# Kernel tuning notes

Hardware: AMD Instinct MI355X
Metric: run time of the kernel (lower is better)

The kernel has to match this reference:

```python
import jax, jax.numpy as jnp
import numpy as np

S = 4096      # total packed sequence length (8 images x 512 patches)
D = 1152      # hidden_dim
H = 16        # num_heads
HD = D // H   # head_dim = 72
MLPD = 4304   # mlp_dim
EPS = 1e-5


def setup_inputs() -> dict:
    key = jax.random.key(0)
    ks = jax.random.split(key, 16)
    f32 = jnp.float32
    w = lambda k, shp: (jax.random.normal(k, shp, f32) * 0.02)
    hidden_states = jax.random.normal(ks[0], (S, D), f32)
    cu_seqlens = (jnp.arange(9, dtype=jnp.int32) * (S // 8))  # [0,512,...,4096]
    angles = jax.random.uniform(ks[1], (S, HD // 2), f32, 0.0, 2.0 * np.pi)
    rope_cos = jnp.cos(angles)
    rope_sin = jnp.sin(angles)
    return {
        "hidden_states": hidden_states,
        "cu_seqlens": cu_seqlens,
        "rope_cos": rope_cos,
        "rope_sin": rope_sin,
        "norm0_scale": jnp.ones((D,), f32),
        "norm0_bias": jnp.zeros((D,), f32),
        "wqkv_w": w(ks[2], (D, 3 * D)),
        "wqkv_b": jnp.zeros((3 * D,), f32),
        "wo_w": w(ks[3], (D, D)),
        "wo_b": jnp.zeros((D,), f32),
        "norm1_scale": jnp.ones((D,), f32),
        "norm1_bias": jnp.zeros((D,), f32),
        "fc0_w": w(ks[4], (D, MLPD)),
        "fc0_b": jnp.zeros((MLPD,), f32),
        "fc1_w": w(ks[5], (MLPD, D)),
        "fc1_b": jnp.zeros((D,), f32),
    }


def _layernorm(x, scale, bias):
    m = jnp.mean(x, axis=-1, keepdims=True)
    v = jnp.mean(jnp.square(x - m), axis=-1, keepdims=True)
    return (x - m) * jax.lax.rsqrt(v + EPS) * scale + bias


def _rope(x, cos, sin):
    # x: (S, H, HD). Complex multiply (x0 + i x1) * (cos + i sin) in real form.
    xr = x.reshape(S, H, HD // 2, 2)
    x0, x1 = xr[..., 0], xr[..., 1]
    c = cos[:, None, :]  # (S, 1, HD/2) broadcast over heads
    s = sin[:, None, :]
    o0 = x0 * c - x1 * s
    o1 = x0 * s + x1 * c
    return jnp.stack([o0, o1], axis=-1).reshape(S, H, HD)


def _block_diag_bias(cu_seqlens):
    positions = jnp.arange(S)
    starts, ends = cu_seqlens[:-1], cu_seqlens[1:]
    in_seg = (positions[:, None] >= starts[None, :]) & (positions[:, None] < ends[None, :])
    seg = jnp.argmax(in_seg.astype(jnp.int32), axis=-1)  # (S,)
    same = seg[:, None] == seg[None, :]
    return jnp.where(same, 0.0, jnp.finfo(jnp.float32).min)  # (S, S)


def reference(hidden_states, cu_seqlens, rope_cos, rope_sin,
              norm0_scale, norm0_bias, wqkv_w, wqkv_b, wo_w, wo_b,
              norm1_scale, norm1_bias, fc0_w, fc0_b, fc1_w, fc1_b):
    # pre-norm attention block
    x = _layernorm(hidden_states, norm0_scale, norm0_bias)
    qkv = (x @ wqkv_w + wqkv_b).reshape(S, 3, H, HD)
    q, k, v = qkv[:, 0], qkv[:, 1], qkv[:, 2]
    q = _rope(q, rope_cos, rope_sin)
    k = _rope(k, rope_cos, rope_sin)
    bias = _block_diag_bias(cu_seqlens)  # (S, S)
    scale = HD ** -0.5
    scores = jnp.einsum('shd,thd->hst', q, k) * scale + bias[None, :, :]
    probs = jax.nn.softmax(scores, axis=-1)
    attn = jnp.einsum('hst,thd->shd', probs, v).reshape(S, D)
    attn = attn @ wo_w + wo_b
    h = hidden_states + attn
    # pre-norm MLP block
    y = _layernorm(h, norm1_scale, norm1_bias)
    y = jax.nn.gelu(y @ fc0_w + fc0_b) @ fc1_w + fc1_b
    return h + y
```

## Files before the change

### kernel.cpp

```cpp
#include <hip/hip_runtime.h>


#define DEV __device__ __forceinline__

typedef __attribute__((ext_vector_type(8))) short short8;
typedef __attribute__((ext_vector_type(4))) float f32x4;

typedef const void __attribute__((address_space(1))) gvoid;
typedef void __attribute__((address_space(3))) lvoid;

DEV ushort f2bf(float f) {
  union { float f; unsigned u; } x; x.f = f;
  unsigned r = (x.u + 0x7FFFu + ((x.u >> 16) & 1u)) >> 16;
  return (ushort)r;
}

DEV float bf2f(ushort u) {
  union { unsigned u; float f; } x; x.u = (unsigned)u << 16;
  return x.f;
}

DEV void gload_lds16(const void* g, void* l) {
  __builtin_amdgcn_global_load_lds((gvoid*)g, (lvoid*)l, 16, 0, 0);
}

DEV f32x4 mfma16(short8 a, short8 b, f32x4 c) {
  return __builtin_amdgcn_mfma_f32_16x16x32_bf16(a, b, c, 0, 0, 0);
}

DEV float gelu_tanh(float x) {
  float x3 = x * x * x;
  return 0.5f * x * (1.f + tanhf(0.7978845608f * (x + 0.044715f * x3)));
}

__global__ void wconv_t(const float* __restrict__ src, ushort* __restrict__ dst,
                        int K, int N, int NP, int KP) {
  __shared__ float tile[32][33];
  const int k0 = blockIdx.x * 32, n0 = blockIdx.y * 32;
  const int tx = threadIdx.x & 31, ty = threadIdx.x >> 5;
#pragma unroll
  for (int i = 0; i < 4; ++i) {
    int r = ty + i * 8;
    float v = 0.f;
    if (k0 + r < K && n0 + tx < N) v = src[(size_t)(k0 + r) * N + n0 + tx];
    tile[tx][r] = v;
  }
  __syncthreads();
#pragma unroll
  for (int i = 0; i < 4; ++i) {
    int r = ty + i * 8;
    dst[(size_t)(n0 + r) * KP + k0 + tx] = f2bf(tile[r][tx]);
  }
}

__global__ __launch_bounds__(256) void ln_bf16(const float* __restrict__ x,
                                               const float* __restrict__ sc,
                                               const float* __restrict__ bi,
                                               ushort* __restrict__ out) {
  const int row = blockIdx.x, tid = threadIdx.x;
  const float* xr = x + (size_t)row * 1152;
  const int n = (tid < 128) ? 5 : 4;
  float vals[5];
  float s = 0.f, s2 = 0.f;
#pragma unroll
  for (int i = 0; i < 5; ++i) {
    if (i < n) { float v = xr[tid + i * 256]; vals[i] = v; s += v; s2 += v * v; }
  }
#pragma unroll
  for (int off = 32; off; off >>= 1) { s += __shfl_xor(s, off); s2 += __shfl_xor(s2, off); }
  __shared__ float rs[4], rs2[4];
  if ((tid & 63) == 0) { rs[tid >> 6] = s; rs2[tid >> 6] = s2; }
  __syncthreads();
  s = rs[0] + rs[1] + rs[2] + rs[3];
  s2 = rs2[0] + rs2[1] + rs2[2] + rs2[3];
  const float mean = s * (1.f / 1152.f);
  const float var = s2 * (1.f / 1152.f) - mean * mean;
  const float rstd = rsqrtf(var + 1e-5f);
  ushort* orow = out + (size_t)row * 1152;
  for (int i = 0; i < n; ++i) {
    int c = tid + i * 256;
    orow[c] = f2bf((vals[i] - mean) * rstd * sc[c] + bi[c]);
  }
}

#define BAR __builtin_amdgcn_s_barrier()
#define LGKM0 do { asm volatile("s_waitcnt lgkmcnt(0)" ::: "memory"); \
                   __builtin_amdgcn_sched_barrier(0); } while (0)
#define VM6 do { asm volatile("s_waitcnt vmcnt(6)" ::: "memory"); \
                 __builtin_amdgcn_sched_barrier(0); } while (0)
#define MMQ(AF, BF, MB, NB)                                                   \
  do {                                                                        \
    __builtin_amdgcn_s_setprio(1);                                            \
    _Pragma("unroll") for (int mf = 0; mf < 4; ++mf)                          \
      _Pragma("unroll") for (int nf = 0; nf < 2; ++nf) {                      \
        acc[(MB) + mf][(NB) + nf] =                                           \
            mfma16(AF[mf][0], BF[nf][0], acc[(MB) + mf][(NB) + nf]);          \
        acc[(MB) + mf][(NB) + nf] =                                           \
            mfma16(AF[mf][1], BF[nf][1], acc[(MB) + mf][(NB) + nf]);          \
      }                                                                       \
    __builtin_amdgcn_s_setprio(0);                                            \
  } while (0)

template <int EPI>
__global__ __launch_bounds__(512, 2) void gemmT(
    const ushort* __restrict__ A, const ushort* __restrict__ Bt,
    const float* __restrict__ bias, const float* __restrict__ resid,
    float* __restrict__ outf, ushort* __restrict__ outh,
    int N, int K, int NT, int n_valid) {
  __shared__ ushort lA[2][256 * 64];
  __shared__ ushort lB[2][256 * 64];
  const int tid = threadIdx.x;
  const int lane = tid & 63, wave = tid >> 6;
  const int l15 = lane & 15, lg = lane >> 4;
  const int wr = wave >> 2, wc = wave & 3;

  const int nx = gridDim.x, ny = gridDim.y;
  const int nwg = nx * ny * gridDim.z;
  int flat = (blockIdx.z * ny + blockIdx.y) * nx + blockIdx.x;
  flat = (flat & 7) * (nwg >> 3) + (flat >> 3);
  const int bx = flat % nx;
  const int rem = flat / nx;
  const int by = rem % ny;
  const int bz = rem / ny;
  const int m0 = by * 256, n0 = bx * 256;
  const int k0 = bz * NT * 64;

  const int rb8 = tid >> 3;
  const int swz = ((tid & 7) ^ (rb8 & 7)) * 8;
  const ushort* Ag = A + (size_t)m0 * K + k0 + swz;
  const ushort* Bg = Bt + (size_t)n0 * K + k0 + swz;
  const int rB = (rb8 & 31) + ((rb8 >> 5) << 6);
  const int rBw = (wave & 3) * 8 + (wave >> 2) * 64;

  auto stA = [&](int b, int u, int t) {
#pragma unroll
    for (int j = 0; j < 2; ++j) {
      const int r = u * 64 + rb8 + j * 128;
      gload_lds16(Ag + (size_t)r * K + t * 64,
                  &lA[b][(u * 64 + wave * 8 + j * 128) * 64]);
    }
  };
  auto stB = [&](int b, int c, int t) {
#pragma unroll
    for (int j = 0; j < 2; ++j) {
      const int r = rB + c * 32 + j * 128;
      gload_lds16(Bg + (size_t)r * K + t * 64,
                  &lB[b][(rBw + c * 32 + j * 128) * 64]);
    }
  };

  const int arow = wr * 128 + l15;
  const int brow = wc * 64 + l15;
  const int cp0 = ((0 + lg) ^ (l15 & 7)) * 8;
  const int cp1 = ((4 + lg) ^ (l15 & 7)) * 8;
  auto rdA = [&](int b, int half, short8 (&a)[4][2]) {
#pragma unroll
    for (int mf = 0; mf < 4; ++mf) {
      const ushort* p = &lA[b][(arow + half * 64 + mf * 16) * 64];
      a[mf][0] = *(const short8*)(p + cp0);
      a[mf][1] = *(const short8*)(p + cp1);
    }
  };
  auto rdB = [&](int b, int h, short8 (&bb)[2][2]) {
#pragma unroll
    for (int nf = 0; nf < 2; ++nf) {
      const ushort* p = &lB[b][(brow + h * 32 + nf * 16) * 64];
      bb[nf][0] = *(const short8*)(p + cp0);
      bb[nf][1] = *(const short8*)(p + cp1);
    }
  };

  f32x4 acc[8][4] = {};
  short8 aL[4][2], aH[4][2], b01[2][2], b23[2][2];

  stA(0, 0, 0); stB(0, 0, 0); stA(0, 1, 0); stB(0, 1, 0);
  stA(1, 0, 1); stB(1, 0, 1); stA(1, 1, 1); stB(1, 1, 1);
  asm volatile("s_waitcnt vmcnt(8)" ::: "memory");
  BAR;
  rdA(0, 0, aL); rdB(0, 0, b01);

  const int NIT = NT >> 1;
  for (int it = 0; it < NIT; ++it) {
    const int tn0 = 2 * it + 2, tn1 = 2 * it + 3;
    const bool more = (it + 1 < NIT);
    rdB(0, 1, b23); if (more) stA(0, 0, tn0);
    BAR; LGKM0; MMQ(aL, b01, 0, 0); BAR;
    rdA(0, 1, aH); if (more) stB(0, 0, tn0);
    BAR; LGKM0; MMQ(aL, b23, 0, 2); BAR;
    if (more) stA(0, 1, tn0);
    BAR; LGKM0; MMQ(aH, b01, 4, 0); VM6; BAR;
    rdA(1, 0, aL); rdB(1, 0, b01); if (more) stB(0, 1, tn0);
    BAR; LGKM0; MMQ(aH, b23, 4, 2); BAR;
    rdB(1, 1, b23); if (more) stA(1, 0, tn1);
    BAR; LGKM0; MMQ(aL, b01, 0, 0); BAR;
    rdA(1, 1, aH); if (more) stB(1, 0, tn1);
    BAR; LGKM0; MMQ(aL, b23, 0, 2); BAR;
    if (more) stA(1, 1, tn1);
    BAR; LGKM0; MMQ(aH, b01, 4, 0); VM6; BAR;
    rdA(0, 0, aL); rdB(0, 0, b01); if (more) stB(1, 1, tn1);
    BAR; LGKM0; MMQ(aH, b23, 4, 2); BAR;
  }

  float* outp = outf;
  if constexpr (EPI == 0) outp = outf + (size_t)bz * 4096 * 1152;
#pragma unroll
  for (int nf = 0; nf < 4; ++nf) {
    const int col = n0 + wc * 64 + nf * 16 + l15;
    if (col >= n_valid) continue;
    const float bv = (EPI != 0) ? bias[col] : 0.f;
#pragma unroll
    for (int mf = 0; mf < 8; ++mf) {
#pragma unroll
      for (int r = 0; r < 4; ++r) {
        const int row = m0 + wr * 128 + mf * 16 + lg * 4 + r;
        const size_t idx = (size_t)row * N + col;
        const float v = acc[mf][nf][r] + bv;
        if constexpr (EPI == 0) outp[idx] = v;
        else if constexpr (EPI == 1) outf[idx] = resid[idx] + v;
        else if constexpr (EPI == 2) outh[idx] = f2bf(gelu_tanh(v));
        else outh[idx] = f2bf(v);
      }
    }
  }
}

__global__ __launch_bounds__(256) void ksum_reduce(
    const float* __restrict__ hb, const float* __restrict__ bias,
    const float* __restrict__ p0, const float* __restrict__ p1,
    float* __restrict__ out) {
  const f32x4* hb4 = (const f32x4*)hb;
  const f32x4* b4 = (const f32x4*)bias;
  const f32x4* p04 = (const f32x4*)p0;
  const f32x4* p14 = (const f32x4*)p1;
  f32x4* o4 = (f32x4*)out;
  const int total = 4096 * 288;
  for (int i = blockIdx.x * 256 + threadIdx.x; i < total; i += gridDim.x * 256)
    o4[i] = hb4[i] + b4[i % 288] + p04[i] + p14[i];
}

__global__ __launch_bounds__(256) void rope_pack(
    const ushort* __restrict__ qkv,
    const float* __restrict__ cosp, const float* __restrict__ sinp,
    ushort* __restrict__ qp, ushort* __restrict__ kp) {
  const int t = blockIdx.x * 256 + threadIdx.x;
  const int c = t % 12;
  const int hs = t / 12;
  const int h = hs & 15;
  const int s = hs >> 4;
  const size_t dst = ((size_t)h * 4096 + s) * 96 + c * 8;
  if (c >= 9) {
    short8 z = {};
    *(short8*)(qp + dst) = z;
    *(short8*)(kp + dst) = z;
    return;
  }
  const size_t base = (size_t)s * 3456 + h * 72 + c * 8;
  const short8 qv = *(const short8*)(qkv + base);
  const short8 kv = *(const short8*)(qkv + base + 1152);
  const f32x4 cs = *(const f32x4*)(cosp + s * 36 + c * 4);
  const f32x4 sn = *(const f32x4*)(sinp + s * 36 + c * 4);
  short8 qo, ko;
#pragma unroll
  for (int j = 0; j < 4; ++j) {
    const float q0 = bf2f((ushort)qv[2 * j]), q1 = bf2f((ushort)qv[2 * j + 1]);
    const float k0 = bf2f((ushort)kv[2 * j]), k1 = bf2f((ushort)kv[2 * j + 1]);
    qo[2 * j] = (short)f2bf((q0 * cs[j] - q1 * sn[j]) * 0.1178511302f);
    qo[2 * j + 1] = (short)f2bf((q0 * sn[j] + q1 * cs[j]) * 0.1178511302f);
    ko[2 * j] = (short)f2bf(k0 * cs[j] - k1 * sn[j]);
    ko[2 * j + 1] = (short)f2bf(k0 * sn[j] + k1 * cs[j]);
  }
  *(short8*)(qp + dst) = qo;
  *(short8*)(kp + dst) = ko;
}

__global__ void v_pack(const ushort* __restrict__ qkv, ushort* __restrict__ vt) {
  __shared__ ushort lv[96][64];
  const int b = blockIdx.x;
  const int h = b >> 6;
  const int s0 = (b & 63) << 6;
  const int tid = threadIdx.x;
#pragma unroll
  for (int it = 0; it < 24; ++it) {
    int idx = tid + it * 256;
    int d = idx % 96, sl = idx / 96;
    lv[d][sl] = (d < 72) ? qkv[(size_t)(s0 + sl) * 3456 + 2304 + h * 72 + d] : (ushort)0;
  }
  __syncthreads();
#pragma unroll
  for (int it = 0; it < 24; ++it) {
    int idx = tid + it * 256;
    int d = idx >> 6, sl = idx & 63;
    vt[((size_t)h * 96 + d) * 4096 + s0 + sl] = lv[d][sl];
  }
}

__global__ __launch_bounds__(256) void attn_kernel(
    const ushort* __restrict__ qp, const ushort* __restrict__ kp,
    const ushort* __restrict__ vt, ushort* __restrict__ attn_out) {
  __shared__ ushort lp[4][16 * 32];
  const int tid = threadIdx.x, lane = tid & 63, wave = tid >> 6;
  const int l15 = lane & 15, lg = lane >> 4;
  const int b = blockIdx.x;
  const int h = b >> 6;
  const int rem = b & 63;
  const int seg = rem >> 3, qt = rem & 7;
  const int q0 = seg * 512 + qt * 64 + wave * 16;

  short8 aq[3];
  const ushort* qrow = qp + ((size_t)h * 4096 + q0 + l15) * 96 + lg * 8;
  aq[0] = *(const short8*)(qrow);
  aq[1] = *(const short8*)(qrow + 32);
  aq[2] = *(const short8*)(qrow + 64);

  f32x4 oacc[5] = {};
  float mrow[4] = {-1e30f, -1e30f, -1e30f, -1e30f};
  float srow[4] = {0.f, 0.f, 0.f, 0.f};

  const ushort* kbase = kp + ((size_t)h * 4096 + seg * 512) * 96;
  const ushort* vbase = vt + (size_t)h * 96 * 4096 + seg * 512;
  ushort* lpw = lp[wave];

  for (int kc = 0; kc < 16; ++kc) {
    f32x4 sc[2] = {};
#pragma unroll
    for (int n = 0; n < 2; ++n) {
      const ushort* krow = kbase + (size_t)(kc * 32 + n * 16 + l15) * 96 + lg * 8;
#pragma unroll
      for (int c = 0; c < 3; ++c) {
        short8 kb = *(const short8*)(krow + c * 32);
        sc[n] = mfma16(aq[c], kb, sc[n]);
      }
    }
    float corr[4];
#pragma unroll
    for (int j = 0; j < 4; ++j) {
      float v = fmaxf(sc[0][j], sc[1][j]);
      v = fmaxf(v, __shfl_xor(v, 1));
      v = fmaxf(v, __shfl_xor(v, 2));
      v = fmaxf(v, __shfl_xor(v, 4));
      v = fmaxf(v, __shfl_xor(v, 8));
      float mn = fmaxf(mrow[j], v);
      corr[j] = __expf(mrow[j] - mn);
      mrow[j] = mn;
    }
    float p0[4], p1[4];
#pragma unroll
    for (int j = 0; j < 4; ++j) {
      p0[j] = __expf(sc[0][j] - mrow[j]);
      p1[j] = __expf(sc[1][j] - mrow[j]);
      float ps = p0[j] + p1[j];
      ps += __shfl_xor(ps, 1);
      ps += __shfl_xor(ps, 2);
      ps += __shfl_xor(ps, 4);
      ps += __shfl_xor(ps, 8);
      srow[j] = srow[j] * corr[j] + ps;
    }
#pragma unroll
    for (int n = 0; n < 5; ++n)
#pragma unroll
      for (int j = 0; j < 4; ++j)
        oacc[n][j] *= corr[j];
#pragma unroll
    for (int j = 0; j < 4; ++j) {
      int row = lg * 4 + j;
      lpw[row * 32 + l15] = f2bf(p0[j]);
      lpw[row * 32 + 16 + l15] = f2bf(p1[j]);
    }
    __syncthreads();
    short8 pa = *(const short8*)&lpw[l15 * 32 + lg * 8];
    const ushort* vrow = vbase + kc * 32 + lg * 8;
#pragma unroll
    for (int n = 0; n < 5; ++n) {
      short8 vb = *(const short8*)(vrow + (size_t)(n * 16 + l15) * 4096);
      oacc[n] = mfma16(pa, vb, oacc[n]);
    }
    __syncthreads();
  }
#pragma unroll
  for (int j = 0; j < 4; ++j) {
    float inv = 1.f / srow[j];
    int row = q0 + lg * 4 + j;
#pragma unroll
    for (int n = 0; n < 5; ++n) {
      int col = n * 16 + l15;
      if (col < 72)
        attn_out[(size_t)row * 1152 + h * 72 + col] = f2bf(oacc[n][j] * inv);
    }
  }
}

extern "C" void kernel_launch(void* const* d_in, const int* in_sizes, int n_in,
                              void* d_out, int out_size, void* d_ws, size_t ws_size,
                              hipStream_t stream) {
  (void)in_sizes; (void)n_in; (void)out_size;
  const float* hidden = (const float*)d_in[0];
  const float* ropec = (const float*)d_in[2];
  const float* ropes = (const float*)d_in[3];
  const float* n0s = (const float*)d_in[4];
  const float* n0b = (const float*)d_in[5];
  const float* wqkv = (const float*)d_in[6];
  const float* bqkv = (const float*)d_in[7];
  const float* wo = (const float*)d_in[8];
  const float* bo = (const float*)d_in[9];
  const float* n1s = (const float*)d_in[10];
  const float* n1b = (const float*)d_in[11];
  const float* wfc0 = (const float*)d_in[12];
  const float* bfc0 = (const float*)d_in[13];
  const float* wfc1 = (const float*)d_in[14];
  const float* bfc1 = (const float*)d_in[15];
  float* out = (float*)d_out;

  char* ws = (char*)d_ws;
  ushort* x_bf   = (ushort*)(ws + 0);
  ushort* wqkv_t = (ushort*)(ws + 9437184);
  ushort* wo_t   = (ushort*)(ws + 17694720);
  ushort* fc0_t  = (ushort*)(ws + 20643840);
  ushort* fc1_t  = (ushort*)(ws + 30670848);
  ushort* qkv_bf = (ushort*)(ws + 41811968);
  ushort* mid    = (ushort*)(ws + 41811968);
  ushort* q_pad  = (ushort*)(ws + 77463552);
  ushort* k_pad  = (ushort*)(ws + 90046464);
  ushort* vt     = (ushort*)(ws + 102629376);
  float*  pbuf   = (float*)(ws + 77463552);
  ushort* attn   = (ushort*)(ws + 115212288);
  float*  hbuf   = (float*)(ws + 124649472);
  ushort* yln    = (ushort*)(ws + 143523840);
  if (ws_size < 152961024) return;

  wconv_t<<<dim3(36, 112), 256, 0, stream>>>(wqkv, wqkv_t, 1152, 3456, 3584, 1152);
  wconv_t<<<dim3(36, 40), 256, 0, stream>>>(wo, wo_t, 1152, 1152, 1280, 1152);
  wconv_t<<<dim3(36, 136), 256, 0, stream>>>(wfc0, fc0_t, 1152, 4304, 4352, 1152);
  wconv_t<<<dim3(136, 40), 256, 0, stream>>>(wfc1, fc1_t, 4304, 1152, 1280, 4352);

  ln_bf16<<<4096, 256, 0, stream>>>(hidden, n0s, n0b, x_bf);

  gemmT<3><<<dim3(14, 16), 512, 0, stream>>>(x_bf, wqkv_t, bqkv, nullptr, nullptr, qkv_bf,
                                             3456, 1152, 18, 3456);
  rope_pack<<<3072, 256, 0, stream>>>(qkv_bf, ropec, ropes, q_pad, k_pad);
  v_pack<<<1024, 256, 0, stream>>>(qkv_bf, vt);

  attn_kernel<<<1024, 256, 0, stream>>>(q_pad, k_pad, vt, attn);

  gemmT<1><<<dim3(5, 16), 512, 0, stream>>>(attn, wo_t, bo, hidden, hbuf, nullptr,
                                            1152, 1152, 18, 1152);
  ln_bf16<<<4096, 256, 0, stream>>>(hbuf, n1s, n1b, yln);

  gemmT<2><<<dim3(17, 16), 512, 0, stream>>>(yln, fc0_t, bfc0, nullptr, nullptr, mid,
                                             4352, 1152, 18, 4304);
  gemmT<0><<<dim3(5, 16, 2), 512, 0, stream>>>(mid, fc1_t, nullptr, nullptr, pbuf, nullptr,
                                               1152, 4352, 34, 1152);
  ksum_reduce<<<2048, 256, 0, stream>>>(hbuf, bfc1, pbuf, pbuf + (size_t)4096 * 1152, out);
}
```

Baseline: 401.3 us.

## Add smaller-tile GEMM kernels for out-proj and MLP layers

Adds two new GEMM kernels. gemmR uses 128x256 tiles, K-step 32 and a 4-buffer LDS pipeline three stages deep; gemm2 uses 128x128 tiles with double buffering. They replace the large-tile gemmT for the output projection, fc0 and split-K fc1. With fewer, larger tiles the old launches left many CUs idle (80 or 272 workgroups), so the smaller tiles are meant to fill the GPU better and cut N-padding waste by shrinking the padded wo/fc1 widths to 1152. The cost is less data reuse per tile and more barriers.

```diff
diff --git a/kernel.cpp b/kernel.cpp
--- a/kernel.cpp
+++ b/kernel.cpp
@@ -224,6 +224,223 @@
   }
 }
 
+template <int EPI>
+__global__ __launch_bounds__(512, 2) void gemmR(
+    const ushort* __restrict__ A, const ushort* __restrict__ Bt,
+    const float* __restrict__ bias, const float* __restrict__ resid,
+    float* __restrict__ outf, ushort* __restrict__ outh,
+    int N, int K, int NT, int n_valid) {
+  __shared__ ushort L[4][12288];
+  const int tid = threadIdx.x;
+  const int lane = tid & 63, wave = tid >> 6;
+  const int l15 = lane & 15, lg = lane >> 4;
+  const int wr = wave >> 2, wc = wave & 3;
+
+  const int nx = gridDim.x, ny = gridDim.y;
+  const int nwg = nx * ny;
+  const int hw = blockIdx.y * nx + blockIdx.x;
+  const int F = (hw & 7) * (nwg >> 3) + (hw >> 3);
+  const int by = F % ny;
+  const int bx = F / ny;
+  const int m0 = by * 128, n0 = bx * 256;
+
+  const ushort* gsrc0;
+  const ushort* gsrc1;
+  const ushort* gsrc2;
+  {
+    int c = tid, r2 = c >> 3, c8 = (c & 7) ^ (r2 & 7);
+    gsrc0 = A + (size_t)(m0 + r2 * 2 + (c8 >> 2)) * K + (c8 & 3) * 8;
+  }
+  {
+    int c = tid, r2 = c >> 3, c8 = (c & 7) ^ (r2 & 7);
+    gsrc1 = Bt + (size_t)(n0 + r2 * 2 + (c8 >> 2)) * K + (c8 & 3) * 8;
+  }
+  {
+    int c = 512 + tid, r2 = c >> 3, c8 = (c & 7) ^ (r2 & 7);
+    gsrc2 = Bt + (size_t)(n0 + r2 * 2 + (c8 >> 2)) * K + (c8 & 3) * 8;
+  }
+  auto stage = [&](int b, int t) {
+    gload_lds16(gsrc0 + t * 32, &L[b][tid * 8]);
+    gload_lds16(gsrc1 + t * 32, &L[b][4096 + tid * 8]);
+    gload_lds16(gsrc2 + t * 32, &L[b][8192 + tid * 8]);
+  };
+
+  int offA[4], offB[4];
+#pragma unroll
+  for (int f = 0; f < 4; ++f) {
+    const int rA = wr * 64 + f * 16 + l15;
+    const int r2 = rA >> 1, c8 = (((rA & 1) << 2) | lg) ^ (r2 & 7);
+    offA[f] = (r2 * 8 + c8) * 8;
+    const int rB = wc * 64 + f * 16 + l15;
+    const int s2 = rB >> 1, d8 = (((rB & 1) << 2) | lg) ^ (s2 & 7);
+    offB[f] = 4096 + (s2 * 8 + d8) * 8;
+  }
+
+  f32x4 acc[4][4] = {};
+  short8 fa0[4], fb0[4], fa1[4], fb1[4];
+
+  stage(0, 0); stage(1, 1); stage(2, 2);
+  asm volatile("s_waitcnt vmcnt(3)" ::: "memory");
+  BAR;
+#pragma unroll
+  for (int f = 0; f < 4; ++f) {
+    fa0[f] = *(const short8*)&L[0][offA[f]];
+    fb0[f] = *(const short8*)&L[0][offB[f]];
+  }
+
+#define RPH(TT, FA, FB, FAN, FBN)                                             \
+  {                                                                           \
+    const int _t = (TT);                                                      \
+    if (_t + 1 < NT) {                                                        \
+      const ushort* _lb = L[(_t + 1) & 3];                                    \
+      _Pragma("unroll") for (int f = 0; f < 4; ++f) {                         \
+        FAN[f] = *(const short8*)&_lb[offA[f]];                               \
+        FBN[f] = *(const short8*)&_lb[offB[f]];                               \
+      }                                                                       \
+    }                                                                         \
+    if (_t + 3 < NT) stage((_t + 3) & 3, _t + 3);                             \
+    BAR;                                                                      \
+    LGKM0;                                                                    \
+    __builtin_amdgcn_s_setprio(1);                                            \
+    _Pragma("unroll") for (int mf = 0; mf < 4; ++mf)                          \
+      _Pragma("unroll") for (int nf = 0; nf < 4; ++nf)                        \
+        acc[mf][nf] = mfma16(FA[mf], FB[nf], acc[mf][nf]);                    \
+    __builtin_amdgcn_s_setprio(0);                                            \
+    if (_t + 3 < NT) { asm volatile("s_waitcnt vmcnt(3)" ::: "memory"); }     \
+    else { asm volatile("s_waitcnt vmcnt(0)" ::: "memory"); }                 \
+    __builtin_amdgcn_sched_barrier(0);                                        \
+    BAR;                                                                      \
+  }
+
+  for (int t = 0; t < NT; t += 2) {
+    RPH(t, fa0, fb0, fa1, fb1);
+    RPH(t + 1, fa1, fb1, fa0, fb0);
+  }
+#undef RPH
+
+  const int cb = n0 + wc * 64 + l15;
+  const int rb = m0 + wr * 64 + lg * 4;
+#pragma unroll
+  for (int j = 0; j < 4; ++j) {
+    const int col = cb + j * 16;
+    const float bv = (col < n_valid) ? bias[col] : 0.f;
+#pragma unroll
+    for (int i = 0; i < 4; ++i) {
+#pragma unroll
+      for (int r = 0; r < 4; ++r) {
+        const int row = rb + i * 16 + r;
+        const size_t idx = (size_t)row * N + col;
+        const float v = acc[i][j][r] + bv;
+        if constexpr (EPI == 1) outf[idx] = resid[idx] + v;
+        else if constexpr (EPI == 2) outh[idx] = f2bf(gelu_tanh(v));
+        else outh[idx] = f2bf(v);
+      }
+    }
+  }
+}
+
+template <int EPI, int BM>
+__global__ __launch_bounds__(BM == 256 ? 512 : 256, 2) void gemm2(
+    const ushort* __restrict__ A, const ushort* __restrict__ Bt,
+    const float* __restrict__ bias, const float* __restrict__ resid,
+    float* __restrict__ outf, ushort* __restrict__ outh,
+    int N, int Kstride, int NT, int n_valid) {
+  constexpr int T = BM * 2;
+  constexpr int NLA = 2;
+  constexpr int NLB = 512 / T;
+  __shared__ ushort lA[2][BM * 32];
+  __shared__ ushort lB[2][128 * 32];
+  const int tid = threadIdx.x;
+  const int lane = tid & 63, wave = tid >> 6;
+  const int l15 = lane & 15, lg = lane >> 4;
+
+  const int nx = gridDim.x, ny = gridDim.y;
+  const int nwg = nx * ny * gridDim.z;
+  const int hw = (blockIdx.z * ny + blockIdx.y) * nx + blockIdx.x;
+  const int F = (hw & 7) * (nwg >> 3) + (hw >> 3);
+  const int by = F % ny;
+  const int C = F / ny;
+  const int bx = C % nx;
+  const int bz = C / nx;
+  const int m0 = by * BM, n0 = bx * 128;
+  const int k0 = bz * NT * 32;
+
+  const int wm = (wave >> 1) * 64;
+  const int wn = (wave & 1) * 64;
+
+  const ushort* Asrc[NLA];
+  const ushort* Bsrc[NLB];
+#pragma unroll
+  for (int i = 0; i < NLA; ++i) {
+    const int c = i * T + tid;
+    const int r = c >> 2, kc = (c & 3) ^ (r & 3);
+    Asrc[i] = A + (size_t)(m0 + r) * Kstride + k0 + kc * 8;
+  }
+#pragma unroll
+  for (int j = 0; j < NLB; ++j) {
+    const int c = j * T + tid;
+    const int r = c >> 2, kc = (c & 3) ^ (r & 3);
+    Bsrc[j] = Bt + (size_t)(n0 + r) * Kstride + k0 + kc * 8;
+  }
+
+  auto stage = [&](int b, int t) {
+#pragma unroll
+    for (int i = 0; i < NLA; ++i)
+      gload_lds16(Asrc[i] + t * 32, &lA[b][(i * T + wave * 64) * 8]);
+#pragma unroll
+    for (int j = 0; j < NLB; ++j)
+      gload_lds16(Bsrc[j] + t * 32, &lB[b][(j * T + wave * 64) * 8]);
+  };
+
+  f32x4 acc[4][4] = {};
+  const int cph = (lg ^ (l15 & 3)) * 8;
+
+  stage(0, 0);
+  __syncthreads();
+  int cur = 0;
+  for (int t = 0; t < NT; ++t) {
+    if (t + 1 < NT) stage(cur ^ 1, t + 1);
+    short8 af[4], bfr[4];
+#pragma unroll
+    for (int i = 0; i < 4; ++i)
+      af[i] = *(const short8*)&lA[cur][(wm + i * 16 + l15) * 32 + cph];
+#pragma unroll
+    for (int j = 0; j < 4; ++j)
+      bfr[j] = *(const short8*)&lB[cur][(wn + j * 16 + l15) * 32 + cph];
+#pragma unroll
+    for (int i = 0; i < 4; ++i)
+#pragma unroll
+      for (int j = 0; j < 4; ++j)
+        acc[i][j] = mfma16(af[i], bfr[j], acc[i][j]);
+    __syncthreads();
+    cur ^= 1;
+  }
+
+  float* outp = outf;
+  if constexpr (EPI == 0) outp = outf + (size_t)bz * 4096 * 1152;
+  const int cb = n0 + wn + l15;
+  const int rb = m0 + wm + lg * 4;
+#pragma unroll
+  for (int j = 0; j < 4; ++j) {
+    const int col = cb + j * 16;
+    const float bv = (EPI != 0 && col < n_valid) ? bias[col] : 0.f;
+    const bool ok = (col < n_valid);
+#pragma unroll
+    for (int i = 0; i < 4; ++i) {
+#pragma unroll
+      for (int r = 0; r < 4; ++r) {
+        const int row = rb + i * 16 + r;
+        const size_t idx = (size_t)row * N + col;
+        const float v = acc[i][j][r] + bv;
+        if constexpr (EPI == 0) outp[idx] = v;
+        else if constexpr (EPI == 1) { if (ok) outf[idx] = resid[idx] + v; }
+        else if constexpr (EPI == 2) outh[idx] = f2bf(gelu_tanh(v));
+        else outh[idx] = f2bf(v);
+      }
+    }
+  }
+}
+
 __global__ __launch_bounds__(256) void ksum_reduce(
     const float* __restrict__ hb, const float* __restrict__ bias,
     const float* __restrict__ p0, const float* __restrict__ p1,
@@ -414,23 +631,23 @@
   ushort* x_bf   = (ushort*)(ws + 0);
   ushort* wqkv_t = (ushort*)(ws + 9437184);
   ushort* wo_t   = (ushort*)(ws + 17694720);
-  ushort* fc0_t  = (ushort*)(ws + 20643840);
-  ushort* fc1_t  = (ushort*)(ws + 30670848);
-  ushort* qkv_bf = (ushort*)(ws + 41811968);
-  ushort* mid    = (ushort*)(ws + 41811968);
-  ushort* q_pad  = (ushort*)(ws + 77463552);
-  ushort* k_pad  = (ushort*)(ws + 90046464);
-  ushort* vt     = (ushort*)(ws + 102629376);
-  float*  pbuf   = (float*)(ws + 77463552);
-  ushort* attn   = (ushort*)(ws + 115212288);
-  float*  hbuf   = (float*)(ws + 124649472);
-  ushort* yln    = (ushort*)(ws + 143523840);
-  if (ws_size < 152961024) return;
+  ushort* fc0_t  = (ushort*)(ws + 20348928);
+  ushort* fc1_t  = (ushort*)(ws + 30375936);
+  ushort* qkv_bf = (ushort*)(ws + 40402944);
+  ushort* mid    = (ushort*)(ws + 40402944);
+  ushort* q_pad  = (ushort*)(ws + 76054528);
+  ushort* k_pad  = (ushort*)(ws + 88637440);
+  ushort* vt     = (ushort*)(ws + 101220352);
+  float*  pbuf   = (float*)(ws + 76054528);
+  ushort* attn   = (ushort*)(ws + 113803264);
+  float*  hbuf   = (float*)(ws + 123240448);
+  ushort* yln    = (ushort*)(ws + 142114816);
+  if (ws_size < 151552000) return;
 
   wconv_t<<<dim3(36, 112), 256, 0, stream>>>(wqkv, wqkv_t, 1152, 3456, 3584, 1152);
-  wconv_t<<<dim3(36, 40), 256, 0, stream>>>(wo, wo_t, 1152, 1152, 1280, 1152);
+  wconv_t<<<dim3(36, 36), 256, 0, stream>>>(wo, wo_t, 1152, 1152, 1152, 1152);
   wconv_t<<<dim3(36, 136), 256, 0, stream>>>(wfc0, fc0_t, 1152, 4304, 4352, 1152);
-  wconv_t<<<dim3(136, 40), 256, 0, stream>>>(wfc1, fc1_t, 4304, 1152, 1280, 4352);
+  wconv_t<<<dim3(136, 36), 256, 0, stream>>>(wfc1, fc1_t, 4304, 1152, 1152, 4352);
 
   ln_bf16<<<4096, 256, 0, stream>>>(hidden, n0s, n0b, x_bf);
 
@@ -441,13 +658,13 @@
 
   attn_kernel<<<1024, 256, 0, stream>>>(q_pad, k_pad, vt, attn);
 
-  gemmT<1><<<dim3(5, 16), 512, 0, stream>>>(attn, wo_t, bo, hidden, hbuf, nullptr,
-                                            1152, 1152, 18, 1152);
+  gemm2<1, 128><<<dim3(9, 32), 256, 0, stream>>>(attn, wo_t, bo, hidden, hbuf, nullptr,
+                                                 1152, 1152, 36, 1152);
   ln_bf16<<<4096, 256, 0, stream>>>(hbuf, n1s, n1b, yln);
 
-  gemmT<2><<<dim3(17, 16), 512, 0, stream>>>(yln, fc0_t, bfc0, nullptr, nullptr, mid,
-                                             4352, 1152, 18, 4304);
-  gemmT<0><<<dim3(5, 16, 2), 512, 0, stream>>>(mid, fc1_t, nullptr, nullptr, pbuf, nullptr,
-                                               1152, 4352, 34, 1152);
+  gemmR<2><<<dim3(17, 32), 512, 0, stream>>>(yln, fc0_t, bfc0, nullptr, nullptr, mid,
+                                             4352, 1152, 36, 4304);
+  gemm2<0, 128><<<dim3(9, 32, 2), 256, 0, stream>>>(mid, fc1_t, nullptr, nullptr, pbuf, nullptr,
+                                                    1152, 4352, 68, 1152);
   ksum_reduce<<<2048, 256, 0, stream>>>(hbuf, bfc1, pbuf, pbuf + (size_t)4096 * 1152, out);
 }
```

Measured after the change: 371.2 us. 1.08x faster.
